# Kernel tuning notes

Measured on AMD Instinct MI355X. Metric: run time of the kernel, lower is better.

## Reference

```python
import jax, jax.numpy as jnp
import numpy as np

N_NODES = 50000
HIDDEN = 128
N_REL = 9
N_LAYERS = 3
N_EDGES = 600000


def setup_inputs() -> dict:
    key = jax.random.key(0)
    k1, k2, k3, k4, k5 = jax.random.split(key, 5)
    edge_index = jax.random.randint(k1, (2, N_EDGES), 0, N_NODES, dtype=jnp.int64 if jax.config.jax_enable_x64 else jnp.int32)
    edge_type = jax.random.randint(k2, (N_EDGES,), 0, N_REL, dtype=edge_index.dtype)
    embeddings = jax.random.uniform(k3, (N_NODES, HIDDEN), dtype=jnp.float32)
    weights = jax.random.uniform(k4, (N_LAYERS, N_REL, HIDDEN, HIDDEN), dtype=jnp.float32)
    biases = jax.random.uniform(k5, (N_LAYERS, N_REL, HIDDEN), dtype=jnp.float32)
    return {"edge_index": edge_index, "edge_type": edge_type,
            "embeddings": embeddings, "weights": weights, "biases": biases}


def reference(edge_index, edge_type, embeddings, weights, biases):
    # RGCN: per relation r, messages = emb[src] @ W[l,r] + b[l,r], scatter-summed
    # into dest. Equivalent vectorized form: precompute X = emb @ W for all
    # relations ([R,N,E]), then a single gather + segment_sum over edges.
    L = weights.shape[0]
    N = embeddings.shape[0]
    dest = edge_index[0]
    src = edge_index[1]
    out = embeddings
    for l in range(L):
        X = jnp.einsum('ne,ref->rnf', out, weights[l])        # [R, N, E]
        msg = X[edge_type, src] + biases[l][edge_type]        # [num_edges, E]
        hidden = jax.ops.segment_sum(msg, dest, num_segments=N)  # [N, E]
        if l + 1 < L:
            hidden = jax.nn.relu(hidden)
        out = hidden
    return out
```

## Files before the change

kernel.cpp:

```cpp
#include <hip/hip_runtime.h>

#define NNODES 50000
#define HID 128
#define NREL 9
#define NLAYERS 3
#define NEDGES 600000

#define NBINS (NREL * NNODES)
#define SCAN_CHUNK 1024
#define NBLK ((NBINS + SCAN_CHUNK - 1) / SCAN_CHUNK)

#define KTOT (NREL * HID)
#define GM2 32
#define KPITCH 1160
#define FPITCH 136

#define HIST_BLKS ((NEDGES + 255) / 256)
#define EMB_BLKS  ((NNODES * HID / 8) / 256)
#define W_BLKS    (NLAYERS * NREL)

typedef __attribute__((ext_vector_type(8))) short short8;
typedef __attribute__((ext_vector_type(4))) float f32x4;

__device__ __forceinline__ short f2bf(float f) {
    union { float f; unsigned u; } c; c.f = f;
    unsigned r = c.u + 0x7fff + ((c.u >> 16) & 1);
    return (short)(r >> 16);
}
__device__ __forceinline__ float bf2f(short v) {
    return __uint_as_float(((unsigned)(unsigned short)v) << 16);
}


__global__ __launch_bounds__(256) void prep_kernel(const int* __restrict__ dst,
                                                   const int* __restrict__ etype,
                                                   int* __restrict__ bins,
                                                   const float* __restrict__ E,
                                                   short* __restrict__ Ebf,
                                                   const float* __restrict__ W,
                                                   short* __restrict__ Wt2) {
    int b = blockIdx.x, tid = threadIdx.x;
    if (b < HIST_BLKS) {
        int e = b * 256 + tid;
        if (e < NEDGES) {
            int bin = etype[e] * NNODES + dst[e];
            atomicAdd(&bins[bin], 1);
        }
    } else if (b < HIST_BLKS + EMB_BLKS) {
        int gid = (b - HIST_BLKS) * 256 + tid;
        const float* p = E + (size_t)gid * 8;
        float4 v0 = *(const float4*)p;
        float4 v1 = *(const float4*)(p + 4);
        short8 o = {f2bf(v0.x), f2bf(v0.y), f2bf(v0.z), f2bf(v0.w),
                    f2bf(v1.x), f2bf(v1.y), f2bf(v1.z), f2bf(v1.w)};
        *(short8*)(Ebf + (size_t)gid * 8) = o;
    } else {
        int lr = b - HIST_BLKS - EMB_BLKS;
        int l = lr / NREL, r = lr - l * NREL;
        const float* w = W + (size_t)lr * HID * HID;
        short* o = Wt2 + (size_t)l * HID * KTOT;
#pragma unroll 4
        for (int i = 0; i < 64; i++) {
            int elem = i * 256 + tid;
            int kk = elem >> 7, n = elem & 127;
            o[(size_t)n * KTOT + r * HID + kk] = f2bf(w[elem]);
        }
    }
}


__global__ __launch_bounds__(256) void scan_pass1(const int* __restrict__ bins,
                                                  int* __restrict__ blocksum) {
    __shared__ int red[256];
    int b = blockIdx.x, t = threadIdx.x;
    int i0 = b * SCAN_CHUNK + t * 4;
    int s = 0;
#pragma unroll
    for (int k = 0; k < 4; k++)
        if (i0 + k < NBINS) s += bins[i0 + k];
    red[t] = s;
    __syncthreads();
    for (int off = 128; off > 0; off >>= 1) {
        if (t < off) red[t] += red[t + off];
        __syncthreads();
    }
    if (t == 0) blocksum[b] = red[0];
}

__global__ __launch_bounds__(512) void scan_pass2(const int* __restrict__ blocksum,
                                                  int* __restrict__ blockoff,
                                                  int* __restrict__ rowptr) {
    __shared__ int s[512];
    int t = threadIdx.x;
    int v = (t < NBLK) ? blocksum[t] : 0;
    s[t] = v;
    __syncthreads();
    for (int off = 1; off < 512; off <<= 1) {
        int x = (t >= off) ? s[t - off] : 0;
        __syncthreads();
        s[t] += x;
        __syncthreads();
    }
    if (t < NBLK) blockoff[t] = s[t] - v;
    if (t == 0) rowptr[NBINS] = NEDGES;
}

__global__ __launch_bounds__(256) void scan_pass3(const int* __restrict__ bins,
                                                  const int* __restrict__ blockoff,
                                                  int* __restrict__ rowptr,
                                                  int* __restrict__ cursor) {
    __shared__ int sc[256];
    int b = blockIdx.x, t = threadIdx.x;
    int i0 = b * SCAN_CHUNK + t * 4;
    int v[4], p[4];
    int s = 0;
#pragma unroll
    for (int k = 0; k < 4; k++) {
        v[k] = (i0 + k < NBINS) ? bins[i0 + k] : 0;
        p[k] = s;
        s += v[k];
    }
    sc[t] = s;
    __syncthreads();
    for (int off = 1; off < 256; off <<= 1) {
        int x = (t >= off) ? sc[t - off] : 0;
        __syncthreads();
        sc[t] += x;
        __syncthreads();
    }
    int base = blockoff[b] + (sc[t] - s);
#pragma unroll
    for (int k = 0; k < 4; k++) {
        if (i0 + k < NBINS) {
            rowptr[i0 + k] = base + p[k];
            cursor[i0 + k] = base + p[k];
        }
    }
}

__global__ void place_kernel(const int* __restrict__ dst, const int* __restrict__ src,
                             const int* __restrict__ etype,
                             int* __restrict__ cursor, int* __restrict__ bsrc) {
    int e = blockIdx.x * blockDim.x + threadIdx.x;
    if (e < NEDGES) {
        int bin = etype[e] * NNODES + dst[e];
        int pos = atomicAdd(&cursor[bin], 1);
        bsrc[pos] = src[e];
    }
}


__global__ __launch_bounds__(256, 2) void fused_kernel(const short* __restrict__ Hin,
                                                       const short* __restrict__ Wt2l,
                                                       const float* __restrict__ Bias,
                                                       const int* __restrict__ rowptr,
                                                       const int* __restrict__ bsrc,
                                                       short* __restrict__ HoutBf,
                                                       float* __restrict__ HoutF,
                                                       int last) {
    __shared__ short As[GM2 * KPITCH];
    __shared__ int   rp_s[NREL * (GM2 + 1)];
    __shared__ float bias_s[NREL * HID];

    int tid  = threadIdx.x;
    int wave = tid >> 6, lane = tid & 63;
    int lm = lane & 15, lq = lane >> 4;
    int row0 = blockIdx.x * GM2;
    int n0   = wave * 32;

    for (int i = tid; i < NREL * (GM2 + 1); i += 256) {
        int r = i / (GM2 + 1), o = i - r * (GM2 + 1);
        int d = row0 + o; if (d > NNODES) d = NNODES;
        rp_s[i] = rowptr[r * NNODES + d];
    }
    for (int i = tid; i < NREL * HID; i += 256) bias_s[i] = Bias[i];
    __syncthreads();

    int team = tid >> 2;
    int cg   = tid & 3;
    int grow = team & 31;
    int nbin = (team < 32) ? 5 : 4;
    int r0g  = (team < 32) ? 0 : 1;
    const short* hb = Hin + cg * 32;

    for (int bj = 0; bj < nbin; bj++) {
        int rr = r0g + bj * 2;
        int rs = rp_s[rr * (GM2 + 1) + grow];
        int re = rp_s[rr * (GM2 + 1) + grow + 1];
        float a[32];
#pragma unroll
        for (int i = 0; i < 32; i++) a[i] = 0.f;

        for (int i = rs; i < re; i += 4) {
            int rem = re - i;
            int i1 = (rem > 1) ? i + 1 : i;
            int i2 = (rem > 2) ? i + 2 : i;
            int i3 = (rem > 3) ? i + 3 : i;
            int s0 = bsrc[i], s1 = bsrc[i1], s2 = bsrc[i2], s3 = bsrc[i3];
            const short8* p0 = (const short8*)(hb + (size_t)s0 * HID);
            const short8* p1 = (const short8*)(hb + (size_t)s1 * HID);
            const short8* p2 = (const short8*)(hb + (size_t)s2 * HID);
            const short8* p3 = (const short8*)(hb + (size_t)s3 * HID);
            short8 v0[4] = {p0[0], p0[1], p0[2], p0[3]};
            short8 v1[4] = {p1[0], p1[1], p1[2], p1[3]};
            short8 v2[4] = {p2[0], p2[1], p2[2], p2[3]};
            short8 v3[4] = {p3[0], p3[1], p3[2], p3[3]};
            float m1 = (rem > 1) ? 1.f : 0.f;
            float m2 = (rem > 2) ? 1.f : 0.f;
            float m3 = (rem > 3) ? 1.f : 0.f;
#pragma unroll
            for (int q = 0; q < 4; q++)
#pragma unroll
                for (int k = 0; k < 8; k++) {
                    float t0 = bf2f(v0[q][k]) + m1 * bf2f(v1[q][k]);
                    float t1 = m2 * bf2f(v2[q][k]) + m3 * bf2f(v3[q][k]);
                    a[q * 8 + k] += t0 + t1;
                }
        }
        short8* ap = (short8*)&As[grow * KPITCH + rr * HID + cg * 32];
#pragma unroll
        for (int q = 0; q < 4; q++) {
            short8 o;
#pragma unroll
            for (int k = 0; k < 8; k++) o[k] = f2bf(a[q * 8 + k]);
            ap[q] = o;
        }
    }
    __syncthreads();

    f32x4 acc[2][2];
#pragma unroll
    for (int a = 0; a < 2; a++)
#pragma unroll
        for (int b = 0; b < 2; b++) acc[a][b] = (f32x4){0.f, 0.f, 0.f, 0.f};

    const short* wb0 = Wt2l + (size_t)(n0 + lm) * KTOT + lq * 8;
    const short* wb1 = wb0 + (size_t)16 * KTOT;

#pragma unroll 4
    for (int kc = 0; kc < KTOT / 32; kc++) {
        short8 b0 = *(const short8*)(wb0 + kc * 32);
        short8 b1 = *(const short8*)(wb1 + kc * 32);
        short8 a0 = *(const short8*)&As[(lm     ) * KPITCH + kc * 32 + lq * 8];
        short8 a1 = *(const short8*)&As[(lm + 16) * KPITCH + kc * 32 + lq * 8];
        __builtin_amdgcn_s_setprio(1);
        acc[0][0] = __builtin_amdgcn_mfma_f32_16x16x32_bf16(a0, b0, acc[0][0], 0, 0, 0);
        acc[1][0] = __builtin_amdgcn_mfma_f32_16x16x32_bf16(a1, b0, acc[1][0], 0, 0, 0);
        acc[0][1] = __builtin_amdgcn_mfma_f32_16x16x32_bf16(a0, b1, acc[0][1], 0, 0, 0);
        acc[1][1] = __builtin_amdgcn_mfma_f32_16x16x32_bf16(a1, b1, acc[1][1], 0, 0, 0);
        __builtin_amdgcn_s_setprio(0);
    }
    __syncthreads();

    if (!last) {
        short (*Et)[FPITCH] = (short(*)[FPITCH])&As[0];
#pragma unroll
        for (int mt = 0; mt < 2; mt++) {
#pragma unroll
            for (int reg = 0; reg < 4; reg++) {
                int rl = mt * 16 + lq * 4 + reg;
                float cr[NREL];
#pragma unroll
                for (int rr = 0; rr < NREL; rr++)
                    cr[rr] = (float)(rp_s[rr * (GM2 + 1) + rl + 1] - rp_s[rr * (GM2 + 1) + rl]);
#pragma unroll
                for (int nt = 0; nt < 2; nt++) {
                    int n = n0 + nt * 16 + lm;
                    float b = 0.f;
#pragma unroll
                    for (int rr = 0; rr < NREL; rr++) b += cr[rr] * bias_s[rr * HID + n];
                    float o = fmaxf(acc[mt][nt][reg] + b, 0.f);
                    Et[rl][n] = f2bf(o);
                }
            }
        }
        __syncthreads();
#pragma unroll
        for (int i = 0; i < 2; i++) {
            int p = i * 256 + tid;
            int row = p >> 4, cc = p & 15;
            int d = row0 + row;
            if (d < NNODES)
                *(short8*)(HoutBf + (size_t)d * HID + cc * 8) = *(const short8*)&Et[row][cc * 8];
        }
    } else {
#pragma unroll
        for (int mt = 0; mt < 2; mt++) {
#pragma unroll
            for (int reg = 0; reg < 4; reg++) {
                int rl = mt * 16 + lq * 4 + reg;
                int d  = row0 + rl;
                if (d >= NNODES) continue;
                float cr[NREL];
#pragma unroll
                for (int rr = 0; rr < NREL; rr++)
                    cr[rr] = (float)(rp_s[rr * (GM2 + 1) + rl + 1] - rp_s[rr * (GM2 + 1) + rl]);
#pragma unroll
                for (int nt = 0; nt < 2; nt++) {
                    int n = n0 + nt * 16 + lm;
                    float b = 0.f;
#pragma unroll
                    for (int rr = 0; rr < NREL; rr++) b += cr[rr] * bias_s[rr * HID + n];
                    HoutF[(size_t)d * HID + n] = acc[mt][nt][reg] + b;
                }
            }
        }
    }
}


extern "C" void kernel_launch(void* const* d_in, const int* in_sizes, int n_in,
                              void* d_out, int out_size, void* d_ws, size_t ws_size,
                              hipStream_t stream) {
    const int*   edge_index = (const int*)d_in[0];
    const int*   etype      = (const int*)d_in[1];
    const float* emb        = (const float*)d_in[2];
    const float* W          = (const float*)d_in[3];
    const float* Bias       = (const float*)d_in[4];
    float*       out        = (float*)d_out;

    const int* dst  = edge_index;
    const int* srcA = edge_index + NEDGES;

    short* Ebf  = (short*)d_ws;
    short* HbfA = Ebf  + (size_t)NNODES * HID;
    short* HbfB = HbfA + (size_t)NNODES * HID;
    short* Wt2  = HbfB + (size_t)NNODES * HID;
    int*   bsrc     = (int*)(Wt2 + (size_t)NLAYERS * HID * KTOT);
    int*   bins     = bsrc + NEDGES + 8;
    int*   cursor   = bins + NBINS;
    int*   rowptr   = cursor + NBINS;
    int*   blocksum = rowptr + NBINS + 1;
    int*   blockoff = blocksum + NBLK;

    hipMemsetAsync(bins, 0, NBINS * sizeof(int), stream);
    prep_kernel<<<HIST_BLKS + EMB_BLKS + W_BLKS, 256, 0, stream>>>(
        dst, etype, bins, emb, Ebf, W, Wt2);
    scan_pass1<<<NBLK, 256, 0, stream>>>(bins, blocksum);
    scan_pass2<<<1, 512, 0, stream>>>(blocksum, blockoff, rowptr);
    scan_pass3<<<NBLK, 256, 0, stream>>>(bins, blockoff, rowptr, cursor);
    place_kernel<<<(NEDGES + 255) / 256, 256, 0, stream>>>(dst, srcA, etype, cursor, bsrc);

    const int nblocks = (NNODES + GM2 - 1) / GM2;
    const short* Hin = Ebf;
    for (int l = 0; l < NLAYERS; l++) {
        int last = (l + 1 == NLAYERS);
        short* Hout = (l == 0) ? HbfA : HbfB;
        if (l == 2) Hout = HbfA;
        const short* Wtl = Wt2 + (size_t)l * HID * KTOT;
        const float* Bl  = Bias + (size_t)l * NREL * HID;
        fused_kernel<<<nblocks, 256, 0, stream>>>(
            Hin, Wtl, Bl, rowptr, bsrc, Hout, out, last);
        Hin = Hout;
    }
}
```

Measured before the change: 492.5 us.

## Reorder edge bins node-major and gather per-node across relations with smaller tiles

Edge bins are now ordered node-major (dst*NREL+etype), so each node's edges across all relations form one contiguous CSR segment. Each team of 16 threads now walks a node's whole segment with 8-edge batched gathers, flushing per-relation slices into shared memory. The old code gathered per (relation, node) bin with 4-way unrolling. The block tile shrinks from 32 to 16 rows and occupancy is raised to 4 blocks per CU. The bias table in shared memory is dropped for direct global reads, and bounds checks go away because 50000 divides evenly by 16. In exchange, each weight fragment is reused over fewer rows and more blocks are launched.

```diff
diff --git a/kernel.cpp b/kernel.cpp
--- a/kernel.cpp
+++ b/kernel.cpp
@@ -11,7 +11,7 @@
 #define NBLK ((NBINS + SCAN_CHUNK - 1) / SCAN_CHUNK)
 
 #define KTOT (NREL * HID)
-#define GM2 32
+#define GM 16
 #define KPITCH 1160
 #define FPITCH 136
 
@@ -43,7 +43,7 @@
     if (b < HIST_BLKS) {
         int e = b * 256 + tid;
         if (e < NEDGES) {
-            int bin = etype[e] * NNODES + dst[e];
+            int bin = dst[e] * NREL + etype[e];
             atomicAdd(&bins[bin], 1);
         }
     } else if (b < HIST_BLKS + EMB_BLKS) {
@@ -142,15 +142,16 @@
                              const int* __restrict__ etype,
                              int* __restrict__ cursor, int* __restrict__ bsrc) {
     int e = blockIdx.x * blockDim.x + threadIdx.x;
+    if (e < 8) bsrc[NEDGES + e] = 0;
     if (e < NEDGES) {
-        int bin = etype[e] * NNODES + dst[e];
+        int bin = dst[e] * NREL + etype[e];
         int pos = atomicAdd(&cursor[bin], 1);
         bsrc[pos] = src[e];
     }
 }
 
 
-__global__ __launch_bounds__(256, 2) void fused_kernel(const short* __restrict__ Hin,
+__global__ __launch_bounds__(256, 4) void fused_kernel(const short* __restrict__ Hin,
                                                        const short* __restrict__ Wt2l,
                                                        const float* __restrict__ Bias,
                                                        const int* __restrict__ rowptr,
@@ -158,81 +159,74 @@
                                                        short* __restrict__ HoutBf,
                                                        float* __restrict__ HoutF,
                                                        int last) {
-    __shared__ short As[GM2 * KPITCH];
-    __shared__ int   rp_s[NREL * (GM2 + 1)];
-    __shared__ float bias_s[NREL * HID];
+    __shared__ short As[GM * KPITCH];
+    __shared__ int   rp_s[GM * NREL + 2];
 
     int tid  = threadIdx.x;
     int wave = tid >> 6, lane = tid & 63;
     int lm = lane & 15, lq = lane >> 4;
-    int row0 = blockIdx.x * GM2;
+    int row0 = blockIdx.x * GM;
     int n0   = wave * 32;
 
-    for (int i = tid; i < NREL * (GM2 + 1); i += 256) {
-        int r = i / (GM2 + 1), o = i - r * (GM2 + 1);
-        int d = row0 + o; if (d > NNODES) d = NNODES;
-        rp_s[i] = rowptr[r * NNODES + d];
-    }
-    for (int i = tid; i < NREL * HID; i += 256) bias_s[i] = Bias[i];
-    __syncthreads();
-
-    int team = tid >> 2;
-    int cg   = tid & 3;
-    int grow = team & 31;
-    int nbin = (team < 32) ? 5 : 4;
-    int r0g  = (team < 32) ? 0 : 1;
-    const short* hb = Hin + cg * 32;
-
-    for (int bj = 0; bj < nbin; bj++) {
-        int rr = r0g + bj * 2;
-        int rs = rp_s[rr * (GM2 + 1) + grow];
-        int re = rp_s[rr * (GM2 + 1) + grow + 1];
-        float a[32];
-#pragma unroll
-        for (int i = 0; i < 32; i++) a[i] = 0.f;
-
-        for (int i = rs; i < re; i += 4) {
-            int rem = re - i;
-            int i1 = (rem > 1) ? i + 1 : i;
-            int i2 = (rem > 2) ? i + 2 : i;
-            int i3 = (rem > 3) ? i + 3 : i;
-            int s0 = bsrc[i], s1 = bsrc[i1], s2 = bsrc[i2], s3 = bsrc[i3];
-            const short8* p0 = (const short8*)(hb + (size_t)s0 * HID);
-            const short8* p1 = (const short8*)(hb + (size_t)s1 * HID);
-            const short8* p2 = (const short8*)(hb + (size_t)s2 * HID);
-            const short8* p3 = (const short8*)(hb + (size_t)s3 * HID);
-            short8 v0[4] = {p0[0], p0[1], p0[2], p0[3]};
-            short8 v1[4] = {p1[0], p1[1], p1[2], p1[3]};
-            short8 v2[4] = {p2[0], p2[1], p2[2], p2[3]};
-            short8 v3[4] = {p3[0], p3[1], p3[2], p3[3]};
-            float m1 = (rem > 1) ? 1.f : 0.f;
-            float m2 = (rem > 2) ? 1.f : 0.f;
-            float m3 = (rem > 3) ? 1.f : 0.f;
-#pragma unroll
-            for (int q = 0; q < 4; q++)
-#pragma unroll
-                for (int k = 0; k < 8; k++) {
-                    float t0 = bf2f(v0[q][k]) + m1 * bf2f(v1[q][k]);
-                    float t1 = m2 * bf2f(v2[q][k]) + m3 * bf2f(v3[q][k]);
-                    a[q * 8 + k] += t0 + t1;
-                }
-        }
-        short8* ap = (short8*)&As[grow * KPITCH + rr * HID + cg * 32];
-#pragma unroll
-        for (int q = 0; q < 4; q++) {
-            short8 o;
-#pragma unroll
-            for (int k = 0; k < 8; k++) o[k] = f2bf(a[q * 8 + k]);
-            ap[q] = o;
-        }
-    }
-    __syncthreads();
-
-    f32x4 acc[2][2];
-#pragma unroll
-    for (int a = 0; a < 2; a++)
-#pragma unroll
-        for (int b = 0; b < 2; b++) acc[a][b] = (f32x4){0.f, 0.f, 0.f, 0.f};
+    for (int i = tid; i < GM * NREL + 2; i += 256) {
+        int g = row0 * NREL + i;
+        rp_s[i] = rowptr[(g < NBINS) ? g : NBINS];
+    }
+    __syncthreads();
+
+    int grow = tid >> 4;
+    int cg   = tid & 15;
+    int rbase = grow * NREL;
+    int rs = rp_s[rbase];
+    int re = rp_s[rbase + NREL];
+    int r  = 0;
+    int rnext = rp_s[rbase + 1];
+    const short* hb = Hin + cg * 8;
+    short* prow = &As[grow * KPITCH + cg * 8];
+
+    float a[8];
+#pragma unroll
+    for (int k = 0; k < 8; k++) a[k] = 0.f;
+
+#define FLUSH_SLICE  {                                                      \
+        short8 o;                                                           \
+        _Pragma("unroll")                                                   \
+        for (int k = 0; k < 8; k++) o[k] = f2bf(a[k]);                      \
+        *(short8*)(prow + r * HID) = o;                                     \
+        _Pragma("unroll")                                                   \
+        for (int k = 0; k < 8; k++) a[k] = 0.f;                             \
+        r++;                                                                \
+        rnext = rp_s[rbase + r + 1];                                        \
+    }
+
+    int j = rs;
+    while (j < re) {
+        int s_[8];
+#pragma unroll
+        for (int t = 0; t < 8; t++) s_[t] = bsrc[j + t];
+        short8 v[8];
+#pragma unroll
+        for (int t = 0; t < 8; t++)
+            v[t] = *(const short8*)(hb + (size_t)s_[t] * HID);
+#pragma unroll
+        for (int t = 0; t < 8; t++) {
+            int jt = j + t;
+            if (jt < re) {
+                while (jt >= rnext) FLUSH_SLICE;
+#pragma unroll
+                for (int k = 0; k < 8; k++) a[k] += bf2f(v[t][k]);
+            }
+        }
+        j += 8;
+    }
+    while (r < NREL) FLUSH_SLICE;
+#undef FLUSH_SLICE
+
+    __syncthreads();
+
+    f32x4 acc[2];
+    acc[0] = (f32x4){0.f, 0.f, 0.f, 0.f};
+    acc[1] = (f32x4){0.f, 0.f, 0.f, 0.f};
 
     const short* wb0 = Wt2l + (size_t)(n0 + lm) * KTOT + lq * 8;
     const short* wb1 = wb0 + (size_t)16 * KTOT;
@@ -241,13 +235,10 @@
     for (int kc = 0; kc < KTOT / 32; kc++) {
         short8 b0 = *(const short8*)(wb0 + kc * 32);
         short8 b1 = *(const short8*)(wb1 + kc * 32);
-        short8 a0 = *(const short8*)&As[(lm     ) * KPITCH + kc * 32 + lq * 8];
-        short8 a1 = *(const short8*)&As[(lm + 16) * KPITCH + kc * 32 + lq * 8];
+        short8 af = *(const short8*)&As[lm * KPITCH + kc * 32 + lq * 8];
         __builtin_amdgcn_s_setprio(1);
-        acc[0][0] = __builtin_amdgcn_mfma_f32_16x16x32_bf16(a0, b0, acc[0][0], 0, 0, 0);
-        acc[1][0] = __builtin_amdgcn_mfma_f32_16x16x32_bf16(a1, b0, acc[1][0], 0, 0, 0);
-        acc[0][1] = __builtin_amdgcn_mfma_f32_16x16x32_bf16(a0, b1, acc[0][1], 0, 0, 0);
-        acc[1][1] = __builtin_amdgcn_mfma_f32_16x16x32_bf16(a1, b1, acc[1][1], 0, 0, 0);
+        acc[0] = __builtin_amdgcn_mfma_f32_16x16x32_bf16(af, b0, acc[0], 0, 0, 0);
+        acc[1] = __builtin_amdgcn_mfma_f32_16x16x32_bf16(af, b1, acc[1], 0, 0, 0);
         __builtin_amdgcn_s_setprio(0);
     }
     __syncthreads();
@@ -255,54 +246,44 @@
     if (!last) {
         short (*Et)[FPITCH] = (short(*)[FPITCH])&As[0];
 #pragma unroll
-        for (int mt = 0; mt < 2; mt++) {
-#pragma unroll
-            for (int reg = 0; reg < 4; reg++) {
-                int rl = mt * 16 + lq * 4 + reg;
-                float cr[NREL];
-#pragma unroll
-                for (int rr = 0; rr < NREL; rr++)
-                    cr[rr] = (float)(rp_s[rr * (GM2 + 1) + rl + 1] - rp_s[rr * (GM2 + 1) + rl]);
-#pragma unroll
-                for (int nt = 0; nt < 2; nt++) {
-                    int n = n0 + nt * 16 + lm;
-                    float b = 0.f;
-#pragma unroll
-                    for (int rr = 0; rr < NREL; rr++) b += cr[rr] * bias_s[rr * HID + n];
-                    float o = fmaxf(acc[mt][nt][reg] + b, 0.f);
-                    Et[rl][n] = f2bf(o);
-                }
+        for (int reg = 0; reg < 4; reg++) {
+            int rl = lq * 4 + reg;
+            float cr[NREL];
+#pragma unroll
+            for (int rr = 0; rr < NREL; rr++)
+                cr[rr] = (float)(rp_s[rl * NREL + rr + 1] - rp_s[rl * NREL + rr]);
+#pragma unroll
+            for (int nt = 0; nt < 2; nt++) {
+                int n = n0 + nt * 16 + lm;
+                float b = 0.f;
+#pragma unroll
+                for (int rr = 0; rr < NREL; rr++) b += cr[rr] * Bias[rr * HID + n];
+                float o = fmaxf(acc[nt][reg] + b, 0.f);
+                Et[rl][n] = f2bf(o);
             }
         }
         __syncthreads();
-#pragma unroll
-        for (int i = 0; i < 2; i++) {
-            int p = i * 256 + tid;
-            int row = p >> 4, cc = p & 15;
+        {
+            int row = tid >> 4, cc = tid & 15;
             int d = row0 + row;
-            if (d < NNODES)
-                *(short8*)(HoutBf + (size_t)d * HID + cc * 8) = *(const short8*)&Et[row][cc * 8];
+            *(short8*)(HoutBf + (size_t)d * HID + cc * 8) = *(const short8*)&Et[row][cc * 8];
         }
     } else {
 #pragma unroll
-        for (int mt = 0; mt < 2; mt++) {
-#pragma unroll
-            for (int reg = 0; reg < 4; reg++) {
-                int rl = mt * 16 + lq * 4 + reg;
-                int d  = row0 + rl;
-                if (d >= NNODES) continue;
-                float cr[NREL];
-#pragma unroll
-                for (int rr = 0; rr < NREL; rr++)
-                    cr[rr] = (float)(rp_s[rr * (GM2 + 1) + rl + 1] - rp_s[rr * (GM2 + 1) + rl]);
-#pragma unroll
-                for (int nt = 0; nt < 2; nt++) {
-                    int n = n0 + nt * 16 + lm;
-                    float b = 0.f;
-#pragma unroll
-                    for (int rr = 0; rr < NREL; rr++) b += cr[rr] * bias_s[rr * HID + n];
-                    HoutF[(size_t)d * HID + n] = acc[mt][nt][reg] + b;
-                }
+        for (int reg = 0; reg < 4; reg++) {
+            int rl = lq * 4 + reg;
+            int d  = row0 + rl;
+            float cr[NREL];
+#pragma unroll
+            for (int rr = 0; rr < NREL; rr++)
+                cr[rr] = (float)(rp_s[rl * NREL + rr + 1] - rp_s[rl * NREL + rr]);
+#pragma unroll
+            for (int nt = 0; nt < 2; nt++) {
+                int n = n0 + nt * 16 + lm;
+                float b = 0.f;
+#pragma unroll
+                for (int rr = 0; rr < NREL; rr++) b += cr[rr] * Bias[rr * HID + n];
+                HoutF[(size_t)d * HID + n] = acc[nt][reg] + b;
             }
         }
     }
@@ -341,7 +322,7 @@
     scan_pass3<<<NBLK, 256, 0, stream>>>(bins, blockoff, rowptr, cursor);
     place_kernel<<<(NEDGES + 255) / 256, 256, 0, stream>>>(dst, srcA, etype, cursor, bsrc);
 
-    const int nblocks = (NNODES + GM2 - 1) / GM2;
+    const int nblocks = NNODES / GM;
     const short* Hin = Ebf;
     for (int l = 0; l < NLAYERS; l++) {
         int last = (l + 1 == NLAYERS);
```

Measured after the change: 548.4 us. 1.11x slower.
